# Performance work log

Measured on AMD Instinct MI355X. Metric: run time of the kernel, lower is better.

The kernel has to match this reference:

```python
import jax, jax.numpy as jnp
import numpy as np

N = 8192          # num_nodes
K = 2             # max_diffusion_step
NUM_SUPPORTS = 2
E = 262144        # edges per support (avg degree 32)
B = 32
INPUT_DIM = 64
HID_DIM = 64
OUTPUT_DIM = 64
NUM_MATRICES = NUM_SUPPORTS * K + 1


def setup_inputs() -> dict:
    key = jax.random.key(0)
    ks = jax.random.split(key, 7)
    inputs = jax.random.normal(ks[0], (B, N * INPUT_DIM), dtype=jnp.float32)
    state = jax.random.normal(ks[1], (B, N * HID_DIM), dtype=jnp.float32)
    support_rows = jax.random.randint(ks[2], (NUM_SUPPORTS, E), 0, N, dtype=jnp.int32)
    support_cols = jax.random.randint(ks[3], (NUM_SUPPORTS, E), 0, N, dtype=jnp.int32)
    # random-walk-like weights, roughly normalized by avg degree
    support_vals = jax.random.uniform(ks[4], (NUM_SUPPORTS, E), dtype=jnp.float32) / 32.0
    fan_in = (INPUT_DIM + HID_DIM) * NUM_MATRICES
    bound = float(np.sqrt(6.0 / (fan_in + OUTPUT_DIM)))  # xavier_uniform
    weight = jax.random.uniform(ks[5], (fan_in, OUTPUT_DIM), dtype=jnp.float32,
                                minval=-bound, maxval=bound)
    biases = jnp.zeros((OUTPUT_DIM,), dtype=jnp.float32)
    return {"inputs": inputs, "state": state, "support_rows": support_rows,
            "support_cols": support_cols, "support_vals": support_vals,
            "weight": weight, "biases": biases}


def _spmm(rows, cols, vals, x2d):
    # sparse [N,N] @ dense [N, D] via gather + segment_sum
    return jax.ops.segment_sum(vals[:, None] * x2d[cols], rows, num_segments=N)


def reference(inputs, state, support_rows, support_cols, support_vals, weight, biases):
    b = inputs.shape[0]
    x0 = jnp.concatenate([inputs.reshape(b, N, -1), state.reshape(b, N, -1)], axis=2)  # [B,N,F]
    f = x0.shape[2]
    # fold batch into the dense dim so each SpMM handles the whole batch at once
    x0_2d = x0.transpose(1, 0, 2).reshape(N, b * f)  # [N, B*F]
    xs = [x0_2d]
    for s in range(NUM_SUPPORTS):
        r, c, v = support_rows[s], support_cols[s], support_vals[s]
        x1 = _spmm(r, c, v, x0_2d)
        xs.append(x1)
        xm2, xm1 = x0_2d, x1
        for _ in range(2, K + 1):
            x2 = 2.0 * _spmm(r, c, v, xm1) - xm2  # Chebyshev recurrence
            xs.append(x2)
            xm2, xm1 = xm1, x2
    m = len(xs)  # == NUM_MATRICES
    x = jnp.stack(xs, axis=0).reshape(m, N, b, f)        # [M,N,B,F]
    x = x.transpose(2, 1, 3, 0).reshape(b * N, f * m)     # matches permute(0,2,3,1).reshape
    out = x @ weight + biases                             # [B*N, output_dim]
    return out.reshape(b, N * weight.shape[1])
```

## Files before the change

### kernel.cpp

```cpp
#include <hip/hip_runtime.h>

#define NN      8192
#define BB      32
#define EE      262144
#define NB      (NN*BB)
#define NS      2

#define BOFF_OUTACC 0
#define BOFF_ZA     67108864
#define BOFF_ZB     100663296
#define BOFF_CSRVAL 134217728
#define BOFF_CSRCOL (BOFF_CSRVAL + 2097152)
#define BOFF_ROWPTR (BOFF_CSRCOL + 2097152)
#define BOFF_CURSOR (BOFF_ROWPTR + 65544)
#define BOFF_COUNTS (BOFF_CURSOR + 65536)

__device__ __forceinline__ unsigned short f2bf(float f) {
    union { float f; unsigned u; } v; v.f = f;
    unsigned r = v.u + 0x7fffu + ((v.u >> 16) & 1u);
    return (unsigned short)(r >> 16);
}
__device__ __forceinline__ float bf_lo(unsigned u) {
    union { unsigned u; float f; } v; v.u = u << 16; return v.f;
}
__device__ __forceinline__ float bf_hi(unsigned u) {
    union { unsigned u; float f; } v; v.u = u & 0xffff0000u; return v.f;
}
__device__ __forceinline__ unsigned packbf(float lo, float hi) {
    return (unsigned)f2bf(lo) | ((unsigned)f2bf(hi) << 16);
}

__global__ __launch_bounds__(256) void hist_kernel(const int* __restrict__ rows,
                                                   int* __restrict__ counts) {
    int idx = blockIdx.x * 256 + threadIdx.x;
    if (idx < NS * EE) {
        int s = idx >> 18;
        int r = rows[idx];
        atomicAdd(&counts[(s << 13) + r], 1);
    }
}

__global__ __launch_bounds__(1024) void scan_kernel(const int* __restrict__ counts,
                                                    int* __restrict__ row_ptr,
                                                    int* __restrict__ cursor) {
    const int s = blockIdx.x;
    const int tid = threadIdx.x;
    __shared__ int part[1024];
    int local[8];
    int sum = 0;
#pragma unroll
    for (int i = 0; i < 8; ++i) {
        local[i] = counts[(s << 13) + tid * 8 + i];
        sum += local[i];
    }
    part[tid] = sum;
    __syncthreads();
    for (int off = 1; off < 1024; off <<= 1) {
        int v = (tid >= off) ? part[tid - off] : 0;
        __syncthreads();
        part[tid] += v;
        __syncthreads();
    }
    int run = (tid == 0) ? 0 : part[tid - 1];
    const int base9 = s * (NN + 1);
    const int base8 = s << 13;
#pragma unroll
    for (int i = 0; i < 8; ++i) {
        row_ptr[base9 + tid * 8 + i] = run;
        cursor[base8 + tid * 8 + i] = run;
        run += local[i];
    }
    if (tid == 1023) row_ptr[base9 + NN] = run;
}

__global__ __launch_bounds__(256) void scatter_kernel(const int* __restrict__ rows,
                                                      const int* __restrict__ cols,
                                                      const float* __restrict__ vals,
                                                      int* __restrict__ cursor,
                                                      int* __restrict__ csr_col,
                                                      float* __restrict__ csr_val) {
    int idx = blockIdx.x * 256 + threadIdx.x;
    if (idx < NS * EE) {
        int s = idx >> 18;
        int r = rows[idx];
        int p = atomicAdd(&cursor[(s << 13) + r], 1);
        csr_col[(s << 18) + p] = cols[idx];
        csr_val[(s << 18) + p] = vals[idx];
    }
}

__global__ __launch_bounds__(256) void gemm_kernel(const float* __restrict__ inputs,
                                                   const float* __restrict__ state,
                                                   const float* __restrict__ weight,
                                                   float* __restrict__ outacc,
                                                   unsigned short* __restrict__ za,
                                                   unsigned short* __restrict__ zb,
                                                   int mstart) {
    __shared__ float At[64][128];
    __shared__ float Wt[64][64];
    const int tid = threadIdx.x;
    const int m = mstart + blockIdx.x;
    const int rowbase = blockIdx.y * 128;
    const int tc = tid & 15;
    const int tr = tid >> 4;

    float4 acc4[8];
#pragma unroll
    for (int i = 0; i < 8; ++i) acc4[i] = make_float4(0.f, 0.f, 0.f, 0.f);

    for (int kt = 0; kt < 2; ++kt) {
        __syncthreads();
        const float* src = kt ? state : inputs;
        {
            const int rloc = tid & 127;
            const int rg = rowbase + rloc;
            const int n = rg >> 5, b = rg & 31;
            const float* srow = src + (size_t)b * (NN * 64) + n * 64;
#pragma unroll
            for (int i = 0; i < 8; ++i) {
                int k4 = i * 2 + (tid >> 7);
                float4 v = *(const float4*)(srow + k4 * 4);
                At[k4 * 4 + 0][rloc] = v.x;
                At[k4 * 4 + 1][rloc] = v.y;
                At[k4 * 4 + 2][rloc] = v.z;
                At[k4 * 4 + 3][rloc] = v.w;
            }
        }
#pragma unroll
        for (int i = 0; i < 4; ++i) {
            int l4 = i * 256 + tid;
            int k = l4 >> 4, o4 = l4 & 15;
            float4 w = *(const float4*)(weight + ((size_t)(kt * 64 + k) * 5 + m) * 64 + o4 * 4);
            *(float4*)&Wt[k][o4 * 4] = w;
        }
        __syncthreads();
#pragma unroll 4
        for (int k = 0; k < 64; ++k) {
            float4 a0 = *(const float4*)&At[k][tr * 8];
            float4 a1 = *(const float4*)&At[k][tr * 8 + 4];
            float4 w = *(const float4*)&Wt[k][tc * 4];
            float af[8] = {a0.x, a0.y, a0.z, a0.w, a1.x, a1.y, a1.z, a1.w};
#pragma unroll
            for (int i = 0; i < 8; ++i) {
                acc4[i].x += af[i] * w.x;
                acc4[i].y += af[i] * w.y;
                acc4[i].z += af[i] * w.z;
                acc4[i].w += af[i] * w.w;
            }
        }
    }
    const int o = tc * 4;
#pragma unroll
    for (int i = 0; i < 8; ++i) {
        int rg = rowbase + tr * 8 + i;
        int n = rg >> 5, b = rg & 31;
        if (m == 0) {
            *(float4*)&outacc[(size_t)n * 2048 + b * 64 + o] = acc4[i];
        } else {
            unsigned short* dst = (m == 1 || m == 3) ? za : zb;
            ushort4 h;
            h.x = f2bf(acc4[i].x); h.y = f2bf(acc4[i].y);
            h.z = f2bf(acc4[i].z); h.w = f2bf(acc4[i].w);
            *(ushort4*)&dst[(size_t)n * 2048 + b * 64 + o] = h;
        }
    }
}

__global__ __launch_bounds__(256) void spmmU_kernel(const int* __restrict__ row_ptr,
                                                    const int* __restrict__ csr_col,
                                                    const float* __restrict__ csr_val,
                                                    unsigned short* __restrict__ za,
                                                    const unsigned short* __restrict__ zb,
                                                    int s) {
    const int r = blockIdx.x;
    const int tid = threadIdx.x;
    const int e0 = row_ptr[s * (NN + 1) + r];
    const int e1 = row_ptr[s * (NN + 1) + r + 1];
    const int* cc = csr_col + (s << 18);
    const float* cv = csr_val + (s << 18);
    const uint4* zbq = (const uint4*)zb;
    float acc[8];
#pragma unroll
    for (int i = 0; i < 8; ++i) acc[i] = 0.f;
    for (int e = e0; e < e1; ++e) {
        int c = cc[e];
        float v = cv[e];
        uint4 x = zbq[(size_t)c * 256 + tid];
        acc[0] += v * bf_lo(x.x); acc[1] += v * bf_hi(x.x);
        acc[2] += v * bf_lo(x.y); acc[3] += v * bf_hi(x.y);
        acc[4] += v * bf_lo(x.z); acc[5] += v * bf_hi(x.z);
        acc[6] += v * bf_lo(x.w); acc[7] += v * bf_hi(x.w);
    }
    uint4* zaq = (uint4*)za;
    uint4 a = zaq[(size_t)r * 256 + tid];
    uint4 outv;
    outv.x = packbf(bf_lo(a.x) + 2.f * acc[0], bf_hi(a.x) + 2.f * acc[1]);
    outv.y = packbf(bf_lo(a.y) + 2.f * acc[2], bf_hi(a.y) + 2.f * acc[3]);
    outv.z = packbf(bf_lo(a.z) + 2.f * acc[4], bf_hi(a.z) + 2.f * acc[5]);
    outv.w = packbf(bf_lo(a.w) + 2.f * acc[6], bf_hi(a.w) + 2.f * acc[7]);
    zaq[(size_t)r * 256 + tid] = outv;
}

__global__ __launch_bounds__(256) void spmmV_kernel(const int* __restrict__ row_ptr,
                                                    const int* __restrict__ csr_col,
                                                    const float* __restrict__ csr_val,
                                                    const unsigned short* __restrict__ vbuf,
                                                    const unsigned short* __restrict__ zb,
                                                    float* __restrict__ outacc,
                                                    int s) {
    const int r = blockIdx.x;
    const int tid = threadIdx.x;
    const int e0 = row_ptr[s * (NN + 1) + r];
    const int e1 = row_ptr[s * (NN + 1) + r + 1];
    const int* cc = csr_col + (s << 18);
    const float* cv = csr_val + (s << 18);
    const uint4* vq = (const uint4*)vbuf;
    float acc[8];
#pragma unroll
    for (int i = 0; i < 8; ++i) acc[i] = 0.f;
    for (int e = e0; e < e1; ++e) {
        int c = cc[e];
        float v = cv[e];
        uint4 x = vq[(size_t)c * 256 + tid];
        acc[0] += v * bf_lo(x.x); acc[1] += v * bf_hi(x.x);
        acc[2] += v * bf_lo(x.y); acc[3] += v * bf_hi(x.y);
        acc[4] += v * bf_lo(x.z); acc[5] += v * bf_hi(x.z);
        acc[6] += v * bf_lo(x.w); acc[7] += v * bf_hi(x.w);
    }
    uint4 t = ((const uint4*)zb)[(size_t)r * 256 + tid];
    float* p = outacc + (size_t)r * 2048 + tid * 8;
    float4 o0 = *(float4*)p, o1 = *(float4*)(p + 4);
    o0.x += acc[0] - bf_lo(t.x); o0.y += acc[1] - bf_hi(t.x);
    o0.z += acc[2] - bf_lo(t.y); o0.w += acc[3] - bf_hi(t.y);
    o1.x += acc[4] - bf_lo(t.z); o1.y += acc[5] - bf_hi(t.z);
    o1.z += acc[6] - bf_lo(t.w); o1.w += acc[7] - bf_hi(t.w);
    *(float4*)p = o0; *(float4*)(p + 4) = o1;
}

__global__ __launch_bounds__(256) void bias_kernel(const float* __restrict__ outacc,
                                                   const float* __restrict__ biases,
                                                   float* __restrict__ out) {
    const int b = blockIdx.y;
    const int n = blockIdx.x * 16 + (threadIdx.x >> 4);
    const int o = (threadIdx.x & 15) * 4;
    float4 v = *(const float4*)(outacc + (size_t)n * 2048 + b * 64 + o);
    float4 bi = *(const float4*)(biases + o);
    v.x += bi.x; v.y += bi.y; v.z += bi.z; v.w += bi.w;
    *(float4*)(out + (size_t)b * (NN * 64) + n * 64 + o) = v;
}

extern "C" void kernel_launch(void* const* d_in, const int* in_sizes, int n_in,
                              void* d_out, int out_size, void* d_ws, size_t ws_size,
                              hipStream_t stream) {
    const float* inputs = (const float*)d_in[0];
    const float* state  = (const float*)d_in[1];
    const int*   rows   = (const int*)d_in[2];
    const int*   cols   = (const int*)d_in[3];
    const float* vals   = (const float*)d_in[4];
    const float* weight = (const float*)d_in[5];
    const float* biases = (const float*)d_in[6];
    float* out = (float*)d_out;

    char* base = (char*)d_ws;
    float*          outacc  = (float*)(base + BOFF_OUTACC);
    unsigned short* za      = (unsigned short*)(base + BOFF_ZA);
    unsigned short* zb      = (unsigned short*)(base + BOFF_ZB);
    float*          csr_val = (float*)(base + BOFF_CSRVAL);
    int*            csr_col = (int*)(base + BOFF_CSRCOL);
    int*            row_ptr = (int*)(base + BOFF_ROWPTR);
    int*            cursor  = (int*)(base + BOFF_CURSOR);
    int*            counts  = (int*)(base + BOFF_COUNTS);

    hipMemsetAsync(counts, 0, NS * NN * sizeof(int), stream);
    hist_kernel<<<(NS * EE + 255) / 256, 256, 0, stream>>>(rows, counts);
    scan_kernel<<<NS, 1024, 0, stream>>>(counts, row_ptr, cursor);
    scatter_kernel<<<(NS * EE + 255) / 256, 256, 0, stream>>>(rows, cols, vals, cursor,
                                                              csr_col, csr_val);

    for (int s = 0; s < NS; ++s) {
        int mstart = (s == 0) ? 0 : 3;
        int mcount = (s == 0) ? 3 : 2;
        gemm_kernel<<<dim3(mcount, NB / 128), 256, 0, stream>>>(inputs, state, weight,
                                                                outacc, za, zb, mstart);
        spmmU_kernel<<<NN, 256, 0, stream>>>(row_ptr, csr_col, csr_val, za, zb, s);
        spmmV_kernel<<<NN, 256, 0, stream>>>(row_ptr, csr_col, csr_val, za, zb,
                                             outacc, s);
    }

    bias_kernel<<<dim3(NN / 16, BB), 256, 0, stream>>>(outacc, biases, out);
}
```

Baseline: 1.075 ms.

## Replace FP32 SIMT projection GEMM with bf16 MFMA kernel using swizzled LDS

```diff
diff --git a/kernel.cpp b/kernel.cpp
--- a/kernel.cpp
+++ b/kernel.cpp
@@ -29,6 +29,9 @@
 __device__ __forceinline__ unsigned packbf(float lo, float hi) {
     return (unsigned)f2bf(lo) | ((unsigned)f2bf(hi) << 16);
 }
+
+typedef __bf16 bf16x8 __attribute__((ext_vector_type(8)));
+typedef float  f32x4  __attribute__((ext_vector_type(4)));
 
 __global__ __launch_bounds__(256) void hist_kernel(const int* __restrict__ rows,
                                                    int* __restrict__ counts) {
@@ -89,79 +92,114 @@
     }
 }
 
-__global__ __launch_bounds__(256) void gemm_kernel(const float* __restrict__ inputs,
-                                                   const float* __restrict__ state,
-                                                   const float* __restrict__ weight,
-                                                   float* __restrict__ outacc,
-                                                   unsigned short* __restrict__ za,
-                                                   unsigned short* __restrict__ zb,
-                                                   int mstart) {
-    __shared__ float At[64][128];
-    __shared__ float Wt[64][64];
+__global__ __launch_bounds__(256) void gemm_mfma_kernel(const float* __restrict__ inputs,
+                                                        const float* __restrict__ state,
+                                                        const float* __restrict__ weight,
+                                                        float* __restrict__ outacc,
+                                                        unsigned short* __restrict__ za,
+                                                        unsigned short* __restrict__ zb,
+                                                        int mstart) {
+    __shared__ unsigned short Abf[128 * 128];
+    __shared__ unsigned short Wt[64 * 128];
     const int tid = threadIdx.x;
     const int m = mstart + blockIdx.x;
     const int rowbase = blockIdx.y * 128;
-    const int tc = tid & 15;
-    const int tr = tid >> 4;
-
-    float4 acc4[8];
-#pragma unroll
-    for (int i = 0; i < 8; ++i) acc4[i] = make_float4(0.f, 0.f, 0.f, 0.f);
-
-    for (int kt = 0; kt < 2; ++kt) {
-        __syncthreads();
-        const float* src = kt ? state : inputs;
-        {
-            const int rloc = tid & 127;
-            const int rg = rowbase + rloc;
-            const int n = rg >> 5, b = rg & 31;
-            const float* srow = src + (size_t)b * (NN * 64) + n * 64;
-#pragma unroll
-            for (int i = 0; i < 8; ++i) {
-                int k4 = i * 2 + (tid >> 7);
-                float4 v = *(const float4*)(srow + k4 * 4);
-                At[k4 * 4 + 0][rloc] = v.x;
-                At[k4 * 4 + 1][rloc] = v.y;
-                At[k4 * 4 + 2][rloc] = v.z;
-                At[k4 * 4 + 3][rloc] = v.w;
+
+    {
+        const int r = tid >> 1, h = tid & 1;
+        const int rg = rowbase + r, n = rg >> 5, b = rg & 31;
+#pragma unroll
+        for (int kt = 0; kt < 2; ++kt) {
+            const float* srow = (kt ? state : inputs) + (size_t)b * (NN * 64) + n * 64 + h * 32;
+            float f[32];
+#pragma unroll
+            for (int j = 0; j < 8; ++j) {
+                float4 v = *(const float4*)(srow + j * 4);
+                f[j * 4 + 0] = v.x; f[j * 4 + 1] = v.y;
+                f[j * 4 + 2] = v.z; f[j * 4 + 3] = v.w;
             }
-        }
-#pragma unroll
-        for (int i = 0; i < 4; ++i) {
-            int l4 = i * 256 + tid;
-            int k = l4 >> 4, o4 = l4 & 15;
-            float4 w = *(const float4*)(weight + ((size_t)(kt * 64 + k) * 5 + m) * 64 + o4 * 4);
-            *(float4*)&Wt[k][o4 * 4] = w;
-        }
-        __syncthreads();
-#pragma unroll 4
-        for (int k = 0; k < 64; ++k) {
-            float4 a0 = *(const float4*)&At[k][tr * 8];
-            float4 a1 = *(const float4*)&At[k][tr * 8 + 4];
-            float4 w = *(const float4*)&Wt[k][tc * 4];
-            float af[8] = {a0.x, a0.y, a0.z, a0.w, a1.x, a1.y, a1.z, a1.w};
-#pragma unroll
-            for (int i = 0; i < 8; ++i) {
-                acc4[i].x += af[i] * w.x;
-                acc4[i].y += af[i] * w.y;
-                acc4[i].z += af[i] * w.z;
-                acc4[i].w += af[i] * w.w;
+#pragma unroll
+            for (int q = 0; q < 4; ++q) {
+                int col8 = kt * 8 + h * 4 + q;
+                uint4 pk;
+                pk.x = packbf(f[q * 8 + 0], f[q * 8 + 1]);
+                pk.y = packbf(f[q * 8 + 2], f[q * 8 + 3]);
+                pk.z = packbf(f[q * 8 + 4], f[q * 8 + 5]);
+                pk.w = packbf(f[q * 8 + 6], f[q * 8 + 7]);
+                *(uint4*)&Abf[r * 128 + ((col8 ^ (r & 7)) * 8)] = pk;
             }
         }
     }
-    const int o = tc * 4;
-#pragma unroll
-    for (int i = 0; i < 8; ++i) {
-        int rg = rowbase + tr * 8 + i;
-        int n = rg >> 5, b = rg & 31;
-        if (m == 0) {
-            *(float4*)&outacc[(size_t)n * 2048 + b * 64 + o] = acc4[i];
-        } else {
-            unsigned short* dst = (m == 1 || m == 3) ? za : zb;
-            ushort4 h;
-            h.x = f2bf(acc4[i].x); h.y = f2bf(acc4[i].y);
-            h.z = f2bf(acc4[i].z); h.w = f2bf(acc4[i].w);
-            *(ushort4*)&dst[(size_t)n * 2048 + b * 64 + o] = h;
+    {
+        const int c = tid & 63, g = tid >> 6;
+        float wf[32];
+#pragma unroll 8
+        for (int i = 0; i < 32; ++i)
+            wf[i] = weight[(size_t)((g * 32 + i) * 5 + m) * 64 + c];
+#pragma unroll
+        for (int q = 0; q < 4; ++q) {
+            int col8 = g * 4 + q;
+            uint4 pk;
+            pk.x = packbf(wf[q * 8 + 0], wf[q * 8 + 1]);
+            pk.y = packbf(wf[q * 8 + 2], wf[q * 8 + 3]);
+            pk.z = packbf(wf[q * 8 + 4], wf[q * 8 + 5]);
+            pk.w = packbf(wf[q * 8 + 6], wf[q * 8 + 7]);
+            *(uint4*)&Wt[c * 128 + ((col8 ^ (c & 7)) * 8)] = pk;
+        }
+    }
+    __syncthreads();
+
+    const int lane = tid & 63;
+    const int wid = tid >> 6;
+    const int g = lane >> 4;
+    const int lr = lane & 15;
+    f32x4 acc[4][2];
+#pragma unroll
+    for (int mi = 0; mi < 4; ++mi)
+#pragma unroll
+        for (int ni = 0; ni < 2; ++ni)
+            acc[mi][ni] = (f32x4){0.f, 0.f, 0.f, 0.f};
+
+#pragma unroll
+    for (int ks = 0; ks < 4; ++ks) {
+        const int col8 = ks * 4 + g;
+        bf16x8 afr[4], bfr[2];
+#pragma unroll
+        for (int mi = 0; mi < 4; ++mi) {
+            int r = (wid >> 1) * 64 + mi * 16 + lr;
+            afr[mi] = *(const bf16x8*)&Abf[r * 128 + ((col8 ^ (r & 7)) * 8)];
+        }
+#pragma unroll
+        for (int ni = 0; ni < 2; ++ni) {
+            int c = (wid & 1) * 32 + ni * 16 + lr;
+            bfr[ni] = *(const bf16x8*)&Wt[c * 128 + ((col8 ^ (c & 7)) * 8)];
+        }
+#pragma unroll
+        for (int mi = 0; mi < 4; ++mi)
+#pragma unroll
+            for (int ni = 0; ni < 2; ++ni)
+                acc[mi][ni] = __builtin_amdgcn_mfma_f32_16x16x32_bf16(
+                    afr[mi], bfr[ni], acc[mi][ni], 0, 0, 0);
+    }
+
+    const int i0 = (lane >> 4) * 4;
+#pragma unroll
+    for (int mi = 0; mi < 4; ++mi) {
+#pragma unroll
+        for (int ni = 0; ni < 2; ++ni) {
+#pragma unroll
+            for (int i = 0; i < 4; ++i) {
+                int row = rowbase + (wid >> 1) * 64 + mi * 16 + i0 + i;
+                int col = (wid & 1) * 32 + ni * 16 + lr;
+                int n = row >> 5, b = row & 31;
+                float v = acc[mi][ni][i];
+                if (m == 0) {
+                    outacc[(size_t)n * 2048 + b * 64 + col] = v;
+                } else {
+                    unsigned short* dst = (m == 1 || m == 3) ? za : zb;
+                    dst[(size_t)n * 2048 + b * 64 + col] = f2bf(v);
+                }
+            }
         }
     }
 }
@@ -280,8 +318,8 @@
     for (int s = 0; s < NS; ++s) {
         int mstart = (s == 0) ? 0 : 3;
         int mcount = (s == 0) ? 3 : 2;
-        gemm_kernel<<<dim3(mcount, NB / 128), 256, 0, stream>>>(inputs, state, weight,
-                                                                outacc, za, zb, mstart);
+        gemm_mfma_kernel<<<dim3(mcount, NB / 128), 256, 0, stream>>>(inputs, state, weight,
+                                                                     outacc, za, zb, mstart);
         spmmU_kernel<<<NN, 256, 0, stream>>>(row_ptr, csr_col, csr_val, za, zb, s);
         spmmV_kernel<<<NN, 256, 0, stream>>>(row_ptr, csr_col, csr_val, za, zb,
                                              outacc, s);
```

Result: slower. 1.100 ms (+2.3%).
